# Kernel optimization log

Hardware: AMD Instinct MI355X
Metric: run time of the kernel (lower is better)

## Reference

```python
import jax, jax.numpy as jnp
import numpy as np

KERNEL = 3          # conv kernel size (stride 1)
NUM_SEG = 512       # static cap on number of pooled segments (pad semantics)
NEG = -10.0         # fill value for positions not covered by the strided conv


def _sinusoidal_pe(S, D):
    pos = np.arange(S)[:, None].astype(np.float32)
    div = np.exp(-np.log(10000.0) * (np.arange(0, D, 2).astype(np.float32) / D))
    pe = np.zeros((S, D), dtype=np.float32)
    pe[:, 0::2] = np.sin(pos * div)
    pe[:, 1::2] = np.cos(pos * div)
    return jnp.asarray(pe)


def setup_inputs() -> dict:
    key = jax.random.key(0)
    B, L, D = 8, 2048, 1024
    Ch = D // KERNEL  # 341
    ks = jax.random.split(key, 4)
    hidden = jax.random.normal(ks[0], (B, L, D), jnp.float32)
    lengths = jax.random.randint(ks[1], (B,), L // 2, L + 1)
    attention_mask = (jnp.arange(L)[None, :] < lengths[:, None]).astype(jnp.float32)
    w1 = jax.random.normal(ks[2], (Ch, D, KERNEL), jnp.float32) / np.sqrt(D * KERNEL)
    b1 = jnp.zeros((Ch,), jnp.float32)
    w2 = jax.random.normal(ks[3], (1, Ch, 1), jnp.float32) / np.sqrt(Ch)
    b2 = jnp.full((1,), -2.5, jnp.float32)  # init_for_12 bias
    return {"hidden": hidden, "attention_mask": attention_mask,
            "w1": w1, "b1": b1, "w2": w2, "b2": b2}


def reference(hidden, attention_mask, w1, b1, w2, b2):
    B, L, D = hidden.shape
    dt = hidden.dtype
    # --- strided-conv boundary logits (eval path, no Gumbel noise) ---
    x = jnp.swapaxes(hidden, 1, 2)  # (B, D, L)
    h = jax.lax.conv_general_dilated(x, w1, (1,), 'VALID',
                                     dimension_numbers=('NCH', 'OIH', 'NCH'))
    h = jax.nn.relu(h + b1[None, :, None])            # (B, Ch, L-2)
    strided = jnp.einsum('bcl,oc->bl', h, w2[:, :, 0]) + b2[0]  # (B, L-2)
    # scatter strided logits to positions kernel-1 + i (i.e. [2:L])
    logits = jnp.full((B, L), NEG, dt).at[:, KERNEL - 1:].set(strided)
    probs = jax.nn.sigmoid(logits)
    soft = probs
    hard_samp = (probs > 0.5).astype(dt)
    hard = hard_samp + soft - jax.lax.stop_gradient(soft)  # straight-through
    # --- mask and force a boundary at the last real token ---
    hard = hard * attention_mask
    pad = attention_mask == 0
    first_pad = pad & (jnp.cumsum(pad.astype(jnp.int32), axis=1) == 1)
    last_real = jnp.roll(first_pad, -1, axis=1).at[:, -1].set(False).astype(dt)
    hard = jnp.maximum(hard, last_real)
    # --- dynamic downsample: mean-pool tokens within boundary segments ---
    seg = jnp.cumsum(hard, axis=1) - hard  # segment id per token (B, L)
    sid = jnp.arange(NUM_SEG, dtype=dt)
    foo = 1.0 - jnp.clip(jnp.abs(sid[None, None, :] - seg[:, :, None]), 0.0, 1.0)  # (B,L,S)
    foo = foo * attention_mask[:, :, None]
    lel = foo / (jnp.sum(foo, axis=1, keepdims=True) + 1e-9)
    pooled = jnp.einsum('bls,bld->bsd', lel, hidden)  # (B, S, D)
    pooled = pooled + _sinusoidal_pe(NUM_SEG, D)[None].astype(dt)
    # --- shortened attention mask (stream compaction of kept positions) ---
    keep = jax.lax.stop_gradient(hard) > 0.5
    order = jnp.argsort(jnp.logical_not(keep).astype(jnp.int32), axis=1)  # stable: kept first
    gathered = jnp.take_along_axis(attention_mask, order, axis=1)[:, :NUM_SEG]
    n_keep = jnp.sum(keep, axis=1)
    valid = jnp.arange(NUM_SEG)[None, :] < n_keep[:, None]
    short_mask = jnp.where(valid, gathered, 0.0)
    num_boundaries = jnp.sum(hard)
    total_positions = jnp.sum(attention_mask)
    return pooled, num_boundaries, total_positions, short_mask
```

## Files before the change

kernel.cpp:

```cpp
#include <hip/hip_runtime.h>
#include <hip/hip_bf16.h>
#include <cmath>

#define B_SZ 8
#define L_SZ 2048
#define D_SZ 1024
#define CH 341
#define CP 384
#define LCONV 2046
#define NSEG 512
#define KDIM 3072
#define KSTEPS 48

#define POOLED_N (B_SZ * NSEG * D_SZ)

typedef _Float16 f16x8 __attribute__((ext_vector_type(8)));
typedef float f32x4 __attribute__((ext_vector_type(4)));

__device__ __forceinline__ void gl_lds16(const void* g, void* l) {
    __builtin_amdgcn_global_load_lds(
        (const __attribute__((address_space(1))) unsigned int*)g,
        (__attribute__((address_space(3))) unsigned int*)l, 16, 0, 0);
}

__global__ __launch_bounds__(256) void convert_hidden_kernel(
        const float* __restrict__ hidden, _Float16* __restrict__ hid16) {
    size_t idx = (size_t)blockIdx.x * 256 + threadIdx.x;
    float4 v0 = ((const float4*)hidden)[idx * 2];
    float4 v1 = ((const float4*)hidden)[idx * 2 + 1];
    f16x8 o;
    o[0] = (_Float16)v0.x; o[1] = (_Float16)v0.y;
    o[2] = (_Float16)v0.z; o[3] = (_Float16)v0.w;
    o[4] = (_Float16)v1.x; o[5] = (_Float16)v1.y;
    o[6] = (_Float16)v1.z; o[7] = (_Float16)v1.w;
    ((f16x8*)hid16)[idx] = o;
}

__global__ __launch_bounds__(256) void convert_w1_kernel(
        const float* __restrict__ w1, const float* __restrict__ b2,
        _Float16* __restrict__ bfrag, float* __restrict__ logits) {
    int idx = blockIdx.x * 256 + threadIdx.x;
    int j = idx & 7;
    int lane = (idx >> 3) & 63;
    int kc = (idx >> 9) & 1;
    int rest = idx >> 10;
    int s = rest % KSTEPS;
    int tt = rest / KSTEPS;
    int c = tt * 16 + (lane & 15);
    int k = s * 64 + kc * 32 + ((lane >> 4) << 3) + j;
    int kk = k >> 10, d = k & 1023;
    float v = (c < CH) ? w1[((size_t)c * 1024 + d) * 3 + kk] : 0.0f;
    bfrag[idx] = (_Float16)v;
    if (idx < B_SZ * LCONV) logits[idx] = b2[0];
}

#define LDS_BUF 8192

__global__ __launch_bounds__(256, 2) void conv_mfma_kernel(
        const _Float16* __restrict__ hid16, const _Float16* __restrict__ bfrag,
        const float* __restrict__ b1, const float* __restrict__ w2,
        float* __restrict__ logits) {
    const int nt = blockIdx.x;
    const int mt = blockIdx.y;
    const int b  = blockIdx.z;
    const int l0 = mt * 64;
    const int n0 = nt * 192;
    const int tid = threadIdx.x;
    const int wave = tid >> 6, lane = tid & 63;
    const int wn = wave;
    const int quad = lane >> 4, l16 = lane & 15;

    __shared__ __align__(16) char lds[2 * LDS_BUF];

    const _Float16* hb = hid16 + (size_t)b * L_SZ * D_SZ;

    const _Float16* pa[2];
    #pragma unroll
    for (int p = 0; p < 2; ++p) {
        int f = p * 256 + tid;
        int kc = f >> 8, e = f & 255;
        int m = ((e >> 6) << 4) + (e & 15);
        int koff = ((e >> 4) & 3) * 8;
        int l = l0 + m; if (l > LCONV - 1) l = LCONV - 1;
        pa[p] = hb + (size_t)l * 1024 + kc * 32 + koff;
    }

    const f16x8* bp = (const f16x8*)bfrag;
    const f16x8* bptr[3];
    #pragma unroll
    for (int jj = 0; jj < 3; ++jj) {
        int tt = nt * 12 + wn * 3 + jj;
        bptr[jj] = bp + (size_t)tt * (KSTEPS * 2 * 64) + lane;
    }

    f32x4 acc[4][3] = {};
    f16x8 bc[3][2], bn[3][2];

    #pragma unroll
    for (int jj = 0; jj < 3; ++jj)
        #pragma unroll
        for (int kc = 0; kc < 2; ++kc)
            bc[jj][kc] = bptr[jj][kc * 64];
    #pragma unroll
    for (int jj = 0; jj < 3; ++jj) bptr[jj] += 128;
    #pragma unroll
    for (int p = 0; p < 2; ++p)
        gl_lds16(pa[p], lds + (p * 256 + wave * 64) * 16);
    #pragma unroll
    for (int p = 0; p < 2; ++p) pa[p] += 64;
    __syncthreads();

    int cur = 0;
    for (int s = 0; s < KSTEPS - 1; ++s) {
        const int nxt = cur ^ LDS_BUF;
        #pragma unroll
        for (int jj = 0; jj < 3; ++jj)
            #pragma unroll
            for (int kc = 0; kc < 2; ++kc)
                bn[jj][kc] = bptr[jj][kc * 64];
        #pragma unroll
        for (int jj = 0; jj < 3; ++jj) bptr[jj] += 128;
        #pragma unroll
        for (int p = 0; p < 2; ++p)
            gl_lds16(pa[p], lds + nxt + (p * 256 + wave * 64) * 16);
        #pragma unroll
        for (int p = 0; p < 2; ++p) pa[p] += 64;

        #pragma unroll
        for (int kc = 0; kc < 2; ++kc) {
            f16x8 a[4];
            #pragma unroll
            for (int ii = 0; ii < 4; ++ii)
                a[ii] = *(const f16x8*)(lds + cur + (kc * 256 + ii * 64 + lane) * 16);
            #pragma unroll
            for (int ii = 0; ii < 4; ++ii)
                #pragma unroll
                for (int jj = 0; jj < 3; ++jj)
                    acc[ii][jj] = __builtin_amdgcn_mfma_f32_16x16x32_f16(
                        a[ii], bc[jj][kc], acc[ii][jj], 0, 0, 0);
        }
        __syncthreads();
        #pragma unroll
        for (int jj = 0; jj < 3; ++jj)
            #pragma unroll
            for (int kc = 0; kc < 2; ++kc)
                bc[jj][kc] = bn[jj][kc];
        cur = nxt;
    }
    #pragma unroll
    for (int kc = 0; kc < 2; ++kc) {
        f16x8 a[4];
        #pragma unroll
        for (int ii = 0; ii < 4; ++ii)
            a[ii] = *(const f16x8*)(lds + cur + (kc * 256 + ii * 64 + lane) * 16);
        #pragma unroll
        for (int ii = 0; ii < 4; ++ii)
            #pragma unroll
            for (int jj = 0; jj < 3; ++jj)
                acc[ii][jj] = __builtin_amdgcn_mfma_f32_16x16x32_f16(
                    a[ii], bc[jj][kc], acc[ii][jj], 0, 0, 0);
    }
    __syncthreads();

    float cb1[3], cw2[3];
    #pragma unroll
    for (int jj = 0; jj < 3; ++jj) {
        int ch = n0 + wn * 48 + jj * 16 + l16;
        bool v = ch < CH;
        cb1[jj] = v ? b1[ch] : 0.0f;
        cw2[jj] = v ? w2[ch] : 0.0f;
    }
    float* red = (float*)lds;
    #pragma unroll
    for (int ii = 0; ii < 4; ++ii)
        #pragma unroll
        for (int r = 0; r < 4; ++r) {
            float P = 0.0f;
            #pragma unroll
            for (int jj = 0; jj < 3; ++jj) {
                float h = acc[ii][jj][r] + cb1[jj];
                if (h > 0.0f) P += h * cw2[jj];
            }
            P += __shfl_xor(P, 1);
            P += __shfl_xor(P, 2);
            P += __shfl_xor(P, 4);
            P += __shfl_xor(P, 8);
            if (l16 == 0)
                red[(ii * 16 + quad * 4 + r) * 4 + wn] = P;
        }
    __syncthreads();
    if (tid < 64) {
        int l = l0 + tid;
        if (l < LCONV)
            atomicAdd(&logits[b * LCONV + l],
                      red[tid * 4] + red[tid * 4 + 1] + red[tid * 4 + 2] + red[tid * 4 + 3]);
    }
}

__global__ __launch_bounds__(256) void fixup_kernel(
        const float* __restrict__ hidden, const float* __restrict__ w1,
        const float* __restrict__ b1, const float* __restrict__ w2,
        const float* __restrict__ b2, float* __restrict__ logits) {
    const int b = blockIdx.y, l0 = blockIdx.x * 64, tid = threadIdx.x;
    __shared__ float hrow[3 * 1024];
    __shared__ float sred[256];
    __shared__ int flags[64];
    __shared__ int nflag;
    if (tid == 0) nflag = 0;
    __syncthreads();
    if (tid < 64) {
        int l = l0 + tid;
        if (l < LCONV) {
            float v = logits[b * LCONV + l];
            if (fabsf(v) < 0.02f) { int k = atomicAdd(&nflag, 1); flags[k] = l; }
        }
    }
    __syncthreads();
    const int nf = nflag;
    for (int fi = 0; fi < nf; ++fi) {
        const int l = flags[fi];
        for (int t = tid; t < 3072; t += 256)
            hrow[t] = hidden[((size_t)b * L_SZ + l) * 1024 + t];
        __syncthreads();
        float tot = 0.0f;
        for (int c = tid; c < CH; c += 256) {
            const float* wr = w1 + (size_t)c * 3072;
            float dot = 0.0f;
            for (int d = 0; d < 1024; ++d)
                dot += hrow[d] * wr[d * 3] + hrow[1024 + d] * wr[d * 3 + 1]
                     + hrow[2048 + d] * wr[d * 3 + 2];
            float h = dot + b1[c];
            if (h > 0.0f) tot += h * w2[c];
        }
        sred[tid] = tot; __syncthreads();
        for (int off = 128; off > 0; off >>= 1) {
            if (tid < off) sred[tid] += sred[tid + off];
            __syncthreads();
        }
        if (tid == 0) logits[b * LCONV + l] = sred[0] + b2[0];
        __syncthreads();
    }
}

__global__ void boundary_scan_kernel(const float* __restrict__ logits,
                                     const float* __restrict__ amask,
                                     int* __restrict__ segstart,
                                     int* __restrict__ segid,
                                     float* __restrict__ out_nb,
                                     float* __restrict__ out_tp,
                                     float* __restrict__ short_mask) {
    const int b = blockIdx.x, tid = threadIdx.x;
    __shared__ int sdata[256];
    __shared__ int s_len, s_total;

    int cnt = 0;
    #pragma unroll
    for (int j = 0; j < 8; ++j) {
        int l = tid * 8 + j;
        cnt += (amask[b * L_SZ + l] > 0.5f) ? 1 : 0;
    }
    sdata[tid] = cnt; __syncthreads();
    for (int off = 128; off > 0; off >>= 1) {
        if (tid < off) sdata[tid] += sdata[tid + off];
        __syncthreads();
    }
    if (tid == 0) s_len = sdata[0];
    __syncthreads();
    const int len = s_len;

    int bits[8]; int tsum = 0;
    #pragma unroll
    for (int j = 0; j < 8; ++j) {
        int l = tid * 8 + j;
        int h = 0;
        if (l >= 2 && l < len) h = (logits[b * LCONV + (l - 2)] > 0.0f) ? 1 : 0;
        if (len < L_SZ && l == len - 1) h = 1;
        bits[j] = h; tsum += h;
    }
    __syncthreads();
    sdata[tid] = tsum; __syncthreads();
    for (int off = 1; off < 256; off <<= 1) {
        int v = (tid >= off) ? sdata[tid - off] : 0;
        __syncthreads();
        sdata[tid] += v;
        __syncthreads();
    }
    const int texcl = sdata[tid] - tsum;
    if (tid == 255) s_total = sdata[255];
    __syncthreads();
    const int total = s_total;

    for (int s = tid; s <= NSEG; s += 256)
        segstart[b * (NSEG + 1) + s] = (s == 0) ? 0 : len;
    __syncthreads();
    int run = texcl;
    #pragma unroll
    for (int j = 0; j < 8; ++j) {
        int l = tid * 8 + j;
        int sv = -1;
        if (l < len && run < NSEG) sv = run;
        segid[b * L_SZ + l] = sv;
        if (bits[j]) {
            if (run + 1 <= NSEG) segstart[b * (NSEG + 1) + run + 1] = l + 1;
            run++;
        }
    }

    if (tid == 0) {
        atomicAdd(out_nb, (float)total);
        atomicAdd(out_tp, (float)len);
    }
    for (int s = tid; s < NSEG; s += 256)
        short_mask[b * NSEG + s] = (s < total) ? 1.0f : 0.0f;
}

__global__ __launch_bounds__(256) void pool_accum_kernel(
        const float* __restrict__ hidden, const int* __restrict__ segid,
        float* __restrict__ pooled) {
    const int chunk = blockIdx.x, b = blockIdx.y;
    const int tid = threadIdx.x;
    const int d0 = tid * 4;
    const int lbase = chunk * 16;
    const float* hb = hidden + (size_t)b * L_SZ * D_SZ + d0;
    const int* sg = segid + b * L_SZ + lbase;
    float4 acc = make_float4(0.f, 0.f, 0.f, 0.f);
    int cur = -1;
    #pragma unroll
    for (int t = 0; t < 16; ++t) {
        int sid = sg[t];
        if (sid != cur) {
            if (cur >= 0) {
                float* dst = pooled + ((size_t)(b * NSEG + cur)) * D_SZ + d0;
                atomicAdd(dst + 0, acc.x); atomicAdd(dst + 1, acc.y);
                atomicAdd(dst + 2, acc.z); atomicAdd(dst + 3, acc.w);
            }
            acc = make_float4(0.f, 0.f, 0.f, 0.f);
            cur = sid;
        }
        if (sid >= 0) {
            float4 v = *(const float4*)(hb + (size_t)(lbase + t) * D_SZ);
            acc.x += v.x; acc.y += v.y; acc.z += v.z; acc.w += v.w;
        }
    }
    if (cur >= 0) {
        float* dst = pooled + ((size_t)(b * NSEG + cur)) * D_SZ + d0;
        atomicAdd(dst + 0, acc.x); atomicAdd(dst + 1, acc.y);
        atomicAdd(dst + 2, acc.z); atomicAdd(dst + 3, acc.w);
    }
}

__global__ __launch_bounds__(256) void pool_final_kernel(
        float* __restrict__ pooled, const int* __restrict__ segstart) {
    const int s = blockIdx.x, b = blockIdx.y, tid = threadIdx.x;
    const int l0 = segstart[b * (NSEG + 1) + s];
    const int l1 = segstart[b * (NSEG + 1) + s + 1];
    const float inv = 1.0f / ((float)(l1 - l0) + 1e-9f);
    const int d0 = tid * 4;
    size_t o = ((size_t)(b * NSEG + s)) * D_SZ + d0;
    float4 v = *(float4*)(pooled + o);
    const float ce = -9.210340371976184f / 512.0f;
    const int i = d0 >> 1;
    const float a0 = (float)s * expf(ce * (float)i);
    const float a1 = (float)s * expf(ce * (float)(i + 1));
    float4 out;
    out.x = v.x * inv + sinf(a0);
    out.y = v.y * inv + cosf(a0);
    out.z = v.z * inv + sinf(a1);
    out.w = v.w * inv + cosf(a1);
    *(float4*)(pooled + o) = out;
}

extern "C" void kernel_launch(void* const* d_in, const int* in_sizes, int n_in,
                              void* d_out, int out_size, void* d_ws, size_t ws_size,
                              hipStream_t stream) {
    const float* hidden = (const float*)d_in[0];
    const float* amask  = (const float*)d_in[1];
    const float* w1     = (const float*)d_in[2];
    const float* b1     = (const float*)d_in[3];
    const float* w2     = (const float*)d_in[4];
    const float* b2     = (const float*)d_in[5];

    float* out    = (float*)d_out;
    float* pooled = out;
    float* nb     = out + POOLED_N;
    float* tp     = nb + 1;
    float* smask  = out + POOLED_N + 2;

    hipMemsetAsync(d_out, 0, (size_t)(POOLED_N + 2) * sizeof(float), stream);

    const size_t HID_E = (size_t)B_SZ * L_SZ * D_SZ;
    const size_t OFF_HID16    = 0;
    const size_t OFF_BPACK    = OFF_HID16 + HID_E * 2;
    const size_t OFF_LOGITS   = OFF_BPACK + (size_t)CP * KDIM * 2;
    const size_t OFF_SEGSTART = OFF_LOGITS + (size_t)B_SZ * LCONV * 4;
    const size_t OFF_SEGID    = OFF_SEGSTART + (size_t)B_SZ * (NSEG + 1) * 4;

    _Float16* hid16  = (_Float16*)((char*)d_ws + OFF_HID16);
    _Float16* bfrag  = (_Float16*)((char*)d_ws + OFF_BPACK);
    float*    logits = (float*)((char*)d_ws + OFF_LOGITS);
    int*      segst  = (int*)((char*)d_ws + OFF_SEGSTART);
    int*      segid  = (int*)((char*)d_ws + OFF_SEGID);

    convert_hidden_kernel<<<(int)(HID_E / 8 / 256), 256, 0, stream>>>(hidden, hid16);
    convert_w1_kernel<<<(CP * KDIM) / 256, 256, 0, stream>>>(w1, b2, bfrag, logits);
    conv_mfma_kernel<<<dim3(2, 32, B_SZ), 256, 0, stream>>>(hid16, bfrag, b1, w2, logits);
    fixup_kernel<<<dim3(32, B_SZ), 256, 0, stream>>>(hidden, w1, b1, w2, b2, logits);
    boundary_scan_kernel<<<B_SZ, 256, 0, stream>>>(logits, amask, segst, segid, nb, tp, smask);
    pool_accum_kernel<<<dim3(128, B_SZ), 256, 0, stream>>>(hidden, segid, pooled);
    pool_final_kernel<<<dim3(NSEG, B_SZ), 256, 0, stream>>>(pooled, segst);
}
```

Measured before the change: 235.1 us.

## Triple-buffer conv MFMA mainloop with explicit vmcnt waits and barriers

The conv GEMM mainloop goes from a double-buffered LDS/register pipeline with __syncthreads each step to a three-stage ring. Three LDS buffers and three B register sets are used, with manual s_waitcnt vmcnt(8) plus s_barrier so two loads stay in flight while one stage is computed. The aim is to hide global-load latency for A (global_load_lds) and B fragments. It raises LDS use to 24KB and register pressure from the extra B set, which could hurt occupancy at launch_bounds(256,2). The handwritten vmcnt counts must match the number of outstanding loads to stay correct.

New measurement: 232.8 us. No clear change (-1.0%).

```diff
diff --git a/kernel.cpp b/kernel.cpp
--- a/kernel.cpp
+++ b/kernel.cpp
@@ -56,6 +56,38 @@
 
 #define LDS_BUF 8192
 
+#define WAITV8() asm volatile("s_waitcnt vmcnt(8)" ::: "memory")
+#define WAITV0() asm volatile("s_waitcnt vmcnt(0)" ::: "memory")
+#define BAR()    __builtin_amdgcn_s_barrier()
+
+#define LOAD_B(DST) do {                                                    \
+    _Pragma("unroll")                                                       \
+    for (int jj = 0; jj < 3; ++jj) {                                        \
+        DST[jj][0] = bptr[jj][0];                                           \
+        DST[jj][1] = bptr[jj][64];                                          \
+        bptr[jj] += 128;                                                    \
+    } } while (0)
+
+#define ISSUE_A(OFF) do {                                                   \
+    gl_lds16(pa0, lds + (OFF) + (wave * 64) * 16);                          \
+    gl_lds16(pa1, lds + (OFF) + (256 + wave * 64) * 16);                    \
+    pa0 += 64; pa1 += 64; } while (0)
+
+#define COMPUTE(OFF, BSET) do {                                             \
+    _Pragma("unroll")                                                       \
+    for (int kc = 0; kc < 2; ++kc) {                                        \
+        f16x8 a[4];                                                         \
+        _Pragma("unroll")                                                   \
+        for (int ii = 0; ii < 4; ++ii)                                      \
+            a[ii] = *(const f16x8*)(lds + (OFF) + (kc * 256 + ii * 64 + lane) * 16); \
+        _Pragma("unroll")                                                   \
+        for (int ii = 0; ii < 4; ++ii)                                      \
+            _Pragma("unroll")                                               \
+            for (int jj = 0; jj < 3; ++jj)                                  \
+                acc[ii][jj] = __builtin_amdgcn_mfma_f32_16x16x32_f16(       \
+                    a[ii], BSET[jj][kc], acc[ii][jj], 0, 0, 0);             \
+    } } while (0)
+
 __global__ __launch_bounds__(256, 2) void conv_mfma_kernel(
         const _Float16* __restrict__ hid16, const _Float16* __restrict__ bfrag,
         const float* __restrict__ b1, const float* __restrict__ w2,
@@ -70,19 +102,23 @@
     const int wn = wave;
     const int quad = lane >> 4, l16 = lane & 15;
 
-    __shared__ __align__(16) char lds[2 * LDS_BUF];
+    __shared__ __align__(16) char lds[3 * LDS_BUF];
 
     const _Float16* hb = hid16 + (size_t)b * L_SZ * D_SZ;
 
-    const _Float16* pa[2];
-    #pragma unroll
-    for (int p = 0; p < 2; ++p) {
-        int f = p * 256 + tid;
-        int kc = f >> 8, e = f & 255;
-        int m = ((e >> 6) << 4) + (e & 15);
-        int koff = ((e >> 4) & 3) * 8;
-        int l = l0 + m; if (l > LCONV - 1) l = LCONV - 1;
-        pa[p] = hb + (size_t)l * 1024 + kc * 32 + koff;
+    const _Float16* pa0;
+    const _Float16* pa1;
+    {
+        int f0 = tid;
+        int m0 = ((f0 >> 6) << 4) + (f0 & 15);
+        int k0 = ((f0 >> 4) & 3) * 8;
+        int l = l0 + m0; if (l > LCONV - 1) l = LCONV - 1;
+        pa0 = hb + (size_t)l * 1024 + k0;
+        int f1 = tid;
+        int m1 = ((f1 >> 6) << 4) + (f1 & 15);
+        int k1 = ((f1 >> 4) & 3) * 8;
+        l = l0 + m1; if (l > LCONV - 1) l = LCONV - 1;
+        pa1 = hb + (size_t)l * 1024 + 32 + k1;
     }
 
     const f16x8* bp = (const f16x8*)bfrag;
@@ -94,72 +130,32 @@
     }
 
     f32x4 acc[4][3] = {};
-    f16x8 bc[3][2], bn[3][2];
-
-    #pragma unroll
-    for (int jj = 0; jj < 3; ++jj)
-        #pragma unroll
-        for (int kc = 0; kc < 2; ++kc)
-            bc[jj][kc] = bptr[jj][kc * 64];
-    #pragma unroll
-    for (int jj = 0; jj < 3; ++jj) bptr[jj] += 128;
-    #pragma unroll
-    for (int p = 0; p < 2; ++p)
-        gl_lds16(pa[p], lds + (p * 256 + wave * 64) * 16);
-    #pragma unroll
-    for (int p = 0; p < 2; ++p) pa[p] += 64;
-    __syncthreads();
-
-    int cur = 0;
-    for (int s = 0; s < KSTEPS - 1; ++s) {
-        const int nxt = cur ^ LDS_BUF;
-        #pragma unroll
-        for (int jj = 0; jj < 3; ++jj)
-            #pragma unroll
-            for (int kc = 0; kc < 2; ++kc)
-                bn[jj][kc] = bptr[jj][kc * 64];
-        #pragma unroll
-        for (int jj = 0; jj < 3; ++jj) bptr[jj] += 128;
-        #pragma unroll
-        for (int p = 0; p < 2; ++p)
-            gl_lds16(pa[p], lds + nxt + (p * 256 + wave * 64) * 16);
-        #pragma unroll
-        for (int p = 0; p < 2; ++p) pa[p] += 64;
-
-        #pragma unroll
-        for (int kc = 0; kc < 2; ++kc) {
-            f16x8 a[4];
-            #pragma unroll
-            for (int ii = 0; ii < 4; ++ii)
-                a[ii] = *(const f16x8*)(lds + cur + (kc * 256 + ii * 64 + lane) * 16);
-            #pragma unroll
-            for (int ii = 0; ii < 4; ++ii)
-                #pragma unroll
-                for (int jj = 0; jj < 3; ++jj)
-                    acc[ii][jj] = __builtin_amdgcn_mfma_f32_16x16x32_f16(
-                        a[ii], bc[jj][kc], acc[ii][jj], 0, 0, 0);
-        }
-        __syncthreads();
-        #pragma unroll
-        for (int jj = 0; jj < 3; ++jj)
-            #pragma unroll
-            for (int kc = 0; kc < 2; ++kc)
-                bc[jj][kc] = bn[jj][kc];
-        cur = nxt;
-    }
-    #pragma unroll
-    for (int kc = 0; kc < 2; ++kc) {
-        f16x8 a[4];
-        #pragma unroll
-        for (int ii = 0; ii < 4; ++ii)
-            a[ii] = *(const f16x8*)(lds + cur + (kc * 256 + ii * 64 + lane) * 16);
-        #pragma unroll
-        for (int ii = 0; ii < 4; ++ii)
-            #pragma unroll
-            for (int jj = 0; jj < 3; ++jj)
-                acc[ii][jj] = __builtin_amdgcn_mfma_f32_16x16x32_f16(
-                    a[ii], bc[jj][kc], acc[ii][jj], 0, 0, 0);
-    }
+    f16x8 B0[3][2], B1[3][2], B2[3][2];
+
+    LOAD_B(B0); ISSUE_A(0);
+    LOAD_B(B1); ISSUE_A(LDS_BUF);
+
+    for (int t = 0; t < 15; ++t) {
+        WAITV8(); BAR();
+        LOAD_B(B2); ISSUE_A(2 * LDS_BUF);
+        COMPUTE(0, B0);
+
+        WAITV8(); BAR();
+        LOAD_B(B0); ISSUE_A(0);
+        COMPUTE(LDS_BUF, B1);
+
+        WAITV8(); BAR();
+        LOAD_B(B1); ISSUE_A(LDS_BUF);
+        COMPUTE(2 * LDS_BUF, B2);
+    }
+    WAITV8(); BAR();
+    LOAD_B(B2); ISSUE_A(2 * LDS_BUF);
+    COMPUTE(0, B0);
+    WAITV8(); BAR();
+    COMPUTE(LDS_BUF, B1);
+    WAITV0(); BAR();
+    COMPUTE(2 * LDS_BUF, B2);
+
     __syncthreads();
 
     float cb1[3], cw2[3];
```
